# Kernel optimization log

Hardware: AMD Instinct MI355X
Metric: run time of the kernel (lower is better)

## Reference

```python
import jax, jax.numpy as jnp
import numpy as np

EMBED_DIM = 1024
NUM_HEADS = 16
HEAD_DIM = EMBED_DIM // NUM_HEADS


def setup_inputs() -> dict:
    key = jax.random.key(0)
    k1, k2, k3, k4, k5 = jax.random.split(key, 5)
    B, T, C = 4, 2048, EMBED_DIM
    scale = 1.0 / np.sqrt(C)
    return {
        "x": jax.random.normal(k1, (B, T, C), dtype=jnp.float32),
        "W_qkv": jax.random.normal(k2, (3 * C, C), dtype=jnp.float32) * scale,
        "b_qkv": jax.random.normal(k3, (3 * C,), dtype=jnp.float32) * 0.02,
        "W_proj": jax.random.normal(k4, (C, C), dtype=jnp.float32) * scale,
        "b_proj": jax.random.normal(k5, (C,), dtype=jnp.float32) * 0.02,
    }


def reference(x, W_qkv, b_qkv, W_proj, b_proj):
    B, T, C = x.shape
    H, D = NUM_HEADS, HEAD_DIM
    qkv = x @ W_qkv.T + b_qkv                      # [B,T,3C]
    q, k, v = jnp.split(qkv, 3, axis=-1)
    q = q.reshape(B, T, H, D).transpose(0, 2, 1, 3)  # [B,H,T,D]
    k = k.reshape(B, T, H, D).transpose(0, 2, 1, 3)
    v = v.reshape(B, T, H, D).transpose(0, 2, 1, 3)
    scores = jnp.einsum("bhqd,bhkd->bhqk", q, k) / np.sqrt(D)  # [B,H,T,T]
    causal = jnp.tril(jnp.ones((T, T), dtype=bool))
    scores = jnp.where(causal, scores, -jnp.inf)
    attn = jax.nn.softmax(scores, axis=-1)
    out = jnp.einsum("bhqk,bhkd->bhqd", attn, v)   # [B,H,T,D]
    out = out.transpose(0, 2, 1, 3).reshape(B, T, C)
    return out @ W_proj.T + b_proj
```

## Files before the change

### kernel.cpp

```cpp
#include <hip/hip_runtime.h>
#include <math.h>

#define EMBED 1024
#define NHEAD 16
#define HDIM  64
#define SEQT  2048
#define BATCH 4

typedef __bf16 bf16x4 __attribute__((ext_vector_type(4)));
typedef __bf16 bf16x8 __attribute__((ext_vector_type(8)));
typedef float  f32x4  __attribute__((ext_vector_type(4)));

#define AS1 __attribute__((address_space(1)))
#define AS3 __attribute__((address_space(3)))
#define GLD_LDS16(gp, lp) __builtin_amdgcn_global_load_lds( \
    (const AS1 unsigned int*)(gp), (AS3 unsigned int*)(lp), 16, 0, 0)

#define QSCALE 0.180336880f

__device__ __forceinline__ unsigned short f2bf_hw(float f) {
    union { __bf16 h; unsigned short u; } c; c.h = (__bf16)f; return c.u;
}

__global__ __launch_bounds__(256)
void cvt_all(const float* __restrict__ x, const float* __restrict__ wq,
             const float* __restrict__ wp,
             unsigned short* __restrict__ xb, unsigned short* __restrict__ wqb,
             unsigned short* __restrict__ wpb)
{
    const int N1 = 2097152;
    const int N2 = 786432;
    int i = blockIdx.x * 256 + threadIdx.x;
    const float4* src; ushort4* dst; int j;
    if (i < N1)            { src = (const float4*)x;  dst = (ushort4*)xb;  j = i; }
    else if (i < N1 + N2)  { src = (const float4*)wq; dst = (ushort4*)wqb; j = i - N1; }
    else                   { src = (const float4*)wp; dst = (ushort4*)wpb; j = i - N1 - N2; }
    float4 v = src[j];
    ushort4 o;
    o.x = f2bf_hw(v.x); o.y = f2bf_hw(v.y); o.z = f2bf_hw(v.z); o.w = f2bf_hw(v.w);
    dst[j] = o;
}

#define BAR do { __builtin_amdgcn_sched_barrier(0); \
                 __builtin_amdgcn_s_barrier(); \
                 __builtin_amdgcn_sched_barrier(0); } while (0)

template<int MODE>
__global__ __launch_bounds__(512, 2)
void gemm_bt_8ph(const unsigned short* __restrict__ A, const unsigned short* __restrict__ Bw,
                 const float* __restrict__ bias,
                 void* out0, void* out1, void* out2,
                 int M, int N, int K)
{
    __shared__ __align__(16) unsigned short Asm[2][256 * 64];
    __shared__ __align__(16) unsigned short Bsm[2][256 * 64];

    const int tid  = threadIdx.x;
    const int lane = tid & 63;
    const int wave = tid >> 6;
    const int wm = wave >> 2, wn = wave & 3;
    const int col = lane & 15, quad = lane >> 4;
    const long m0 = (long)blockIdx.y * 256, n0 = (long)blockIdx.x * 256;

    f32x4 acc[8][4];
#pragma unroll
    for (int mi = 0; mi < 8; mi++)
#pragma unroll
        for (int ni = 0; ni < 4; ni++) acc[mi][ni] = (f32x4){0.f, 0.f, 0.f, 0.f};

    const int srow  = tid >> 3;
    const int sslot = tid & 7;
    const int gslot = sslot ^ (srow & 7);
    const unsigned short* Agb = A  + (m0 + srow) * (long)K + gslot * 8;
    const unsigned short* Bgb = Bw + (n0 + srow) * (long)K + gslot * 8;

#define STAGE(b, kt_) do { const long ko_ = (long)(kt_) * 64; \
    _Pragma("unroll") for (int r_ = 0; r_ < 4; r_++) { \
        GLD_LDS16(Agb + (long)r_ * 64 * K + ko_, &Asm[b][0] + r_ * 4096 + tid * 8); \
        GLD_LDS16(Bgb + (long)r_ * 64 * K + ko_, &Bsm[b][0] + r_ * 4096 + tid * 8); \
    } } while (0)

#define LOAD_A(qm_) do { _Pragma("unroll") for (int i_ = 0; i_ < 4; i_++) { \
        const int row_ = wm * 128 + ((qm_) * 4 + i_) * 16 + col; \
        const int rx_ = row_ & 7; \
        af[i_][0] = *(const bf16x8*)&Ac[row_ * 64 + ((quad    ) ^ rx_) * 8]; \
        af[i_][1] = *(const bf16x8*)&Ac[row_ * 64 + ((quad + 4) ^ rx_) * 8]; \
    } } while (0)

#define LOAD_B(qn_) do { _Pragma("unroll") for (int j_ = 0; j_ < 2; j_++) { \
        const int row_ = wn * 64 + ((qn_) * 2 + j_) * 16 + col; \
        const int rx_ = row_ & 7; \
        bfv[j_][0] = *(const bf16x8*)&Bc[row_ * 64 + ((quad    ) ^ rx_) * 8]; \
        bfv[j_][1] = *(const bf16x8*)&Bc[row_ * 64 + ((quad + 4) ^ rx_) * 8]; \
    } } while (0)

#define MFMA_Q(qm_, qn_) do { __builtin_amdgcn_s_setprio(1); \
    _Pragma("unroll") for (int i_ = 0; i_ < 4; i_++) \
    _Pragma("unroll") for (int j_ = 0; j_ < 2; j_++) { \
        acc[(qm_) * 4 + i_][(qn_) * 2 + j_] = __builtin_amdgcn_mfma_f32_16x16x32_bf16( \
            af[i_][0], bfv[j_][0], acc[(qm_) * 4 + i_][(qn_) * 2 + j_], 0, 0, 0); \
        acc[(qm_) * 4 + i_][(qn_) * 2 + j_] = __builtin_amdgcn_mfma_f32_16x16x32_bf16( \
            af[i_][1], bfv[j_][1], acc[(qm_) * 4 + i_][(qn_) * 2 + j_], 0, 0, 0); \
    } \
    __builtin_amdgcn_s_setprio(0); } while (0)

    STAGE(0, 0);
    __builtin_amdgcn_s_waitcnt(0x0F70);
    BAR;

    const int T = K >> 6;
    for (int kt = 0; kt < T; kt++) {
        const int cur = kt & 1;
        const unsigned short* Ac = &Asm[cur][0];
        const unsigned short* Bc = &Bsm[cur][0];
        bf16x8 af[4][2], bfv[2][2];

        LOAD_A(0); LOAD_B(0);
        if (kt + 1 < T) STAGE(cur ^ 1, kt + 1);
        BAR;
        MFMA_Q(0, 0);
        BAR;
        LOAD_B(1);
        BAR;
        MFMA_Q(0, 1);
        BAR;
        LOAD_A(1);
        BAR;
        MFMA_Q(1, 1);
        BAR;
        LOAD_B(0);
        BAR;
        MFMA_Q(1, 0);
        __builtin_amdgcn_s_waitcnt(0x0F70);
        BAR;
    }

#undef STAGE
#undef LOAD_A
#undef LOAD_B
#undef MFMA_Q

#pragma unroll
    for (int mi = 0; mi < 8; mi++) {
#pragma unroll
        for (int ni = 0; ni < 4; ni++) {
            long n = n0 + wn * 64 + ni * 16 + col;
            float bv = bias[n];
#pragma unroll
            for (int r = 0; r < 4; r++) {
                long m = m0 + wm * 128 + mi * 16 + quad * 4 + r;
                float v = acc[mi][ni][r] + bv;
                if (MODE == 0) {
                    ((float*)out0)[m * N + n] = v;
                } else {
                    int which = (int)(n >> 10);
                    int c = (int)(n & 1023);
                    int h = c >> 6, d = c & 63;
                    int b = (int)(m >> 11), t = (int)(m & 2047);
                    long bh = (long)(b * NHEAD + h);
                    if (which == 0)      ((unsigned short*)out0)[(bh * SEQT + t) * HDIM + d] = f2bf_hw(v * QSCALE);
                    else if (which == 1) ((unsigned short*)out1)[(bh * SEQT + t) * HDIM + d] = f2bf_hw(v);
                    else                 ((unsigned short*)out2)[(bh * HDIM + d) * SEQT + t] = f2bf_hw(v);
                }
            }
        }
    }
}

#define PPAD 72

__global__ __launch_bounds__(256, 3)
void flash_attn_mfma4(const unsigned short* __restrict__ Qb,
                      const unsigned short* __restrict__ Kb,
                      const unsigned short* __restrict__ Vt,
                      unsigned short* __restrict__ Ob)
{
    __shared__ __align__(16) unsigned short P_lds[128 * PPAD];
    __shared__ __align__(16) unsigned short K_lds[2][64 * 64];
    __shared__ __align__(16) unsigned short V_lds[2][64 * 64];
    __shared__ __align__(16) float L_lds[128];

    const int tid  = threadIdx.x;
    const int lane = tid & 63;
    const int wave = tid >> 6;
    const int col  = lane & 15;
    const int quad = lane >> 4;

    const int idx = blockIdx.x;
    const int qt = 15 - (idx >> 6);
    const int hb = idx & 63;
    const int h = hb & 15, b = hb >> 4;
    const int q0 = qt * 128;
    const long bh = (long)(b * NHEAD + h);
    const unsigned short* Kbh = Kb + bh * SEQT * HDIM;
    const unsigned short* Vbh = Vt + bh * HDIM * SEQT;
    const int ktiles = 2 * qt + 2;

    const int r0 = tid >> 3,         c0 = (tid & 7) ^ (r0 & 7);
    const int r1 = (tid + 256) >> 3, c1 = (tid & 7) ^ (r1 & 7);

    bf16x8 qf[2][2];
#pragma unroll
    for (int ni = 0; ni < 2; ni++) {
        const unsigned short* qrow = Qb + (bh * SEQT + q0 + wave * 32 + ni * 16 + col) * HDIM;
        qf[ni][0] = *(const bf16x8*)(qrow + quad * 8);
        qf[ni][1] = *(const bf16x8*)(qrow + 32 + quad * 8);
    }

    GLD_LDS16(Kbh + r0 * HDIM + c0 * 8,        &K_lds[0][0] + tid * 8);
    GLD_LDS16(Kbh + r1 * HDIM + c1 * 8,        &K_lds[0][0] + 2048 + tid * 8);
    GLD_LDS16(Vbh + (long)r0 * SEQT + c0 * 8,  &V_lds[0][0] + tid * 8);
    GLD_LDS16(Vbh + (long)r1 * SEQT + c1 * 8,  &V_lds[0][0] + 2048 + tid * 8);

    f32x4 o[2][4];
#pragma unroll
    for (int mi = 0; mi < 2; mi++)
#pragma unroll
        for (int dt = 0; dt < 4; dt++) o[mi][dt] = (f32x4){0.f, 0.f, 0.f, 0.f};
    float rs[2] = {0.f, 0.f};

    const int cswz0 = quad ^ (col & 7);
    const int cswz1 = (quad + 4) ^ (col & 7);

    for (int kt = 0; kt < ktiles; kt++) {
        const int cur = kt & 1;
        __builtin_amdgcn_s_waitcnt(0x0F70);
        __syncthreads();
        if (kt + 1 < ktiles) {
            const int k0n = (kt + 1) * 64, nxt = cur ^ 1;
            GLD_LDS16(Kbh + (k0n + r0) * HDIM + c0 * 8,       &K_lds[nxt][0] + tid * 8);
            GLD_LDS16(Kbh + (k0n + r1) * HDIM + c1 * 8,       &K_lds[nxt][0] + 2048 + tid * 8);
            GLD_LDS16(Vbh + (long)r0 * SEQT + k0n + c0 * 8,   &V_lds[nxt][0] + tid * 8);
            GLD_LDS16(Vbh + (long)r1 * SEQT + k0n + c1 * 8,   &V_lds[nxt][0] + 2048 + tid * 8);
        }

        const unsigned short* Kc = &K_lds[cur][0];
        f32x4 st[4][2];
#pragma unroll
        for (int mt = 0; mt < 4; mt++) {
            const int row = mt * 16 + col;
            bf16x8 kf0 = *(const bf16x8*)&Kc[row * 64 + cswz0 * 8];
            bf16x8 kf1 = *(const bf16x8*)&Kc[row * 64 + cswz1 * 8];
#pragma unroll
            for (int ni = 0; ni < 2; ni++) {
                f32x4 acc = (f32x4){0.f, 0.f, 0.f, 0.f};
                acc = __builtin_amdgcn_mfma_f32_16x16x32_bf16(kf0, qf[ni][0], acc, 0, 0, 0);
                acc = __builtin_amdgcn_mfma_f32_16x16x32_bf16(kf1, qf[ni][1], acc, 0, 0, 0);
                st[mt][ni] = acc;
            }
        }
        const int k0 = kt * 64;
        if (kt >= 2 * qt) {
#pragma unroll
            for (int mt = 0; mt < 4; mt++) {
                const int keybase = k0 + mt * 16 + quad * 4;
#pragma unroll
                for (int ni = 0; ni < 2; ni++) {
                    const int qg = q0 + wave * 32 + ni * 16 + col;
#pragma unroll
                    for (int r = 0; r < 4; r++)
                        if (keybase + r > qg) st[mt][ni][r] = -INFINITY;
                }
            }
        }

#pragma unroll
        for (int mt = 0; mt < 4; mt++)
#pragma unroll
            for (int ni = 0; ni < 2; ni++) {
                f32x4 p;
#pragma unroll
                for (int r = 0; r < 4; r++) p[r] = __builtin_amdgcn_exp2f(st[mt][ni][r]);
                rs[ni] += (p[0] + p[1]) + (p[2] + p[3]);
                bf16x4 pb = __builtin_convertvector(p, bf16x4);
                *(bf16x4*)&P_lds[(wave * 32 + ni * 16 + col) * PPAD + mt * 16 + quad * 4] = pb;
            }

        const unsigned short* Vc = &V_lds[cur][0];
#pragma unroll
        for (int mi = 0; mi < 2; mi++) {
            const unsigned short* prow = &P_lds[(wave * 32 + mi * 16 + col) * PPAD];
            bf16x8 pf0 = *(const bf16x8*)(prow + quad * 8);
            bf16x8 pf1 = *(const bf16x8*)(prow + 32 + quad * 8);
#pragma unroll
            for (int dt = 0; dt < 4; dt++) {
                const int row = dt * 16 + col;
                bf16x8 vf0 = *(const bf16x8*)&Vc[row * 64 + cswz0 * 8];
                bf16x8 vf1 = *(const bf16x8*)&Vc[row * 64 + cswz1 * 8];
                o[mi][dt] = __builtin_amdgcn_mfma_f32_16x16x32_bf16(pf0, vf0, o[mi][dt], 0, 0, 0);
                o[mi][dt] = __builtin_amdgcn_mfma_f32_16x16x32_bf16(pf1, vf1, o[mi][dt], 0, 0, 0);
            }
        }
    }

#pragma unroll
    for (int ni = 0; ni < 2; ni++) {
        rs[ni] += __shfl_xor(rs[ni], 16);
        rs[ni] += __shfl_xor(rs[ni], 32);
        if (quad == 0) L_lds[wave * 32 + ni * 16 + col] = rs[ni];
    }
    __syncthreads();
    f32x4 lf[2];
#pragma unroll
    for (int mi = 0; mi < 2; mi++)
        lf[mi] = *(const f32x4*)&L_lds[wave * 32 + mi * 16 + quad * 4];

#pragma unroll
    for (int mi = 0; mi < 2; mi++)
#pragma unroll
        for (int r = 0; r < 4; r++) {
            float inv = 1.f / lf[mi][r];
            int t = q0 + wave * 32 + mi * 16 + quad * 4 + r;
            unsigned short* orow = Ob + ((long)(b * SEQT + t)) * EMBED + h * HDIM;
#pragma unroll
            for (int dt = 0; dt < 4; dt++)
                orow[dt * 16 + col] = f2bf_hw(o[mi][dt][r] * inv);
        }
}

extern "C" void kernel_launch(void* const* d_in, const int* in_sizes, int n_in,
                              void* d_out, int out_size, void* d_ws, size_t ws_size,
                              hipStream_t stream)
{
    const float* x     = (const float*)d_in[0];
    const float* Wqkv  = (const float*)d_in[1];
    const float* bqkv  = (const float*)d_in[2];
    const float* Wproj = (const float*)d_in[3];
    const float* bproj = (const float*)d_in[4];
    float* out = (float*)d_out;

    const long Mbt = (long)BATCH * SEQT;
    const long per = (long)BATCH * NHEAD * SEQT * HDIM;

    unsigned short* xb  = (unsigned short*)d_ws;
    unsigned short* wqb = xb  + per;
    unsigned short* wpb = wqb + 3 * EMBED * EMBED;
    unsigned short* Qb  = wpb + EMBED * EMBED;
    unsigned short* Kb  = Qb + per;
    unsigned short* Vt  = Kb + per;
    unsigned short* Ob  = Vt + per;

    cvt_all<<<12288, 256, 0, stream>>>(x, Wqkv, Wproj, xb, wqb, wpb);

    dim3 g1(3 * EMBED / 256, Mbt / 256);
    gemm_bt_8ph<1><<<g1, 512, 0, stream>>>(xb, wqb, bqkv, Qb, Kb, Vt,
                                           (int)Mbt, 3 * EMBED, EMBED);

    flash_attn_mfma4<<<1024, 256, 0, stream>>>(Qb, Kb, Vt, Ob);

    dim3 g3(EMBED / 256, Mbt / 256);
    gemm_bt_8ph<0><<<g3, 512, 0, stream>>>(Ob, wpb, bproj, out, nullptr, nullptr,
                                           (int)Mbt, EMBED, EMBED);
}
```

Before: 284.2 us.

## Rework GEMM as triple-buffered 256x128 tile pipeline with XCD-aware block remap

```diff
diff --git a/kernel.cpp b/kernel.cpp
--- a/kernel.cpp
+++ b/kernel.cpp
@@ -47,24 +47,32 @@
 
 template<int MODE>
 __global__ __launch_bounds__(512, 2)
-void gemm_bt_8ph(const unsigned short* __restrict__ A, const unsigned short* __restrict__ Bw,
-                 const float* __restrict__ bias,
-                 void* out0, void* out1, void* out2,
-                 int M, int N, int K)
+void gemm_bt_pipe(const unsigned short* __restrict__ A, const unsigned short* __restrict__ Bw,
+                  const float* __restrict__ bias,
+                  void* out0, void* out1, void* out2,
+                  int M, int N)
 {
-    __shared__ __align__(16) unsigned short Asm[2][256 * 64];
-    __shared__ __align__(16) unsigned short Bsm[2][256 * 64];
+    const int K = 1024;
+    const int T = 16;
+    __shared__ __align__(16) unsigned short Asm[3][256 * 64];
+    __shared__ __align__(16) unsigned short Bsm[3][128 * 64];
 
     const int tid  = threadIdx.x;
     const int lane = tid & 63;
     const int wave = tid >> 6;
-    const int wm = wave >> 2, wn = wave & 3;
+    const int wm = wave >> 1, wn = wave & 1;
     const int col = lane & 15, quad = lane >> 4;
-    const long m0 = (long)blockIdx.y * 256, n0 = (long)blockIdx.x * 256;
-
-    f32x4 acc[8][4];
-#pragma unroll
-    for (int mi = 0; mi < 8; mi++)
+
+    const int gx = gridDim.x;
+    const int nwg = gx * gridDim.y;
+    int wg = blockIdx.y * gx + blockIdx.x;
+    wg = (wg & 7) * (nwg >> 3) + (wg >> 3);
+    const long m0 = (long)(wg / gx) * 256;
+    const long n0 = (long)(wg % gx) * 128;
+
+    f32x4 acc[4][4];
+#pragma unroll
+    for (int mi = 0; mi < 4; mi++)
 #pragma unroll
         for (int ni = 0; ni < 4; ni++) acc[mi][ni] = (f32x4){0.f, 0.f, 0.f, 0.f};
 
@@ -74,81 +82,80 @@
     const unsigned short* Agb = A  + (m0 + srow) * (long)K + gslot * 8;
     const unsigned short* Bgb = Bw + (n0 + srow) * (long)K + gslot * 8;
 
-#define STAGE(b, kt_) do { const long ko_ = (long)(kt_) * 64; \
-    _Pragma("unroll") for (int r_ = 0; r_ < 4; r_++) { \
+#define STAGE_A(b, t_) do { const long ko_ = (long)(t_) * 64; \
+    _Pragma("unroll") for (int r_ = 0; r_ < 4; r_++) \
         GLD_LDS16(Agb + (long)r_ * 64 * K + ko_, &Asm[b][0] + r_ * 4096 + tid * 8); \
+    } while (0)
+#define STAGE_B(b, t_) do { const long ko_ = (long)(t_) * 64; \
+    _Pragma("unroll") for (int r_ = 0; r_ < 2; r_++) \
         GLD_LDS16(Bgb + (long)r_ * 64 * K + ko_, &Bsm[b][0] + r_ * 4096 + tid * 8); \
-    } } while (0)
-
-#define LOAD_A(qm_) do { _Pragma("unroll") for (int i_ = 0; i_ < 4; i_++) { \
-        const int row_ = wm * 128 + ((qm_) * 4 + i_) * 16 + col; \
+    } while (0)
+
+#define LOAD_A() do { _Pragma("unroll") for (int i_ = 0; i_ < 4; i_++) { \
+        const int row_ = wm * 64 + i_ * 16 + col; \
         const int rx_ = row_ & 7; \
         af[i_][0] = *(const bf16x8*)&Ac[row_ * 64 + ((quad    ) ^ rx_) * 8]; \
         af[i_][1] = *(const bf16x8*)&Ac[row_ * 64 + ((quad + 4) ^ rx_) * 8]; \
     } } while (0)
 
 #define LOAD_B(qn_) do { _Pragma("unroll") for (int j_ = 0; j_ < 2; j_++) { \
-        const int row_ = wn * 64 + ((qn_) * 2 + j_) * 16 + col; \
+        const int row_ = wn * 64 + (qn_) * 32 + j_ * 16 + col; \
         const int rx_ = row_ & 7; \
         bfv[j_][0] = *(const bf16x8*)&Bc[row_ * 64 + ((quad    ) ^ rx_) * 8]; \
         bfv[j_][1] = *(const bf16x8*)&Bc[row_ * 64 + ((quad + 4) ^ rx_) * 8]; \
     } } while (0)
 
-#define MFMA_Q(qm_, qn_) do { __builtin_amdgcn_s_setprio(1); \
+#define MFMA_Q(qn_) do { __builtin_amdgcn_s_setprio(1); \
     _Pragma("unroll") for (int i_ = 0; i_ < 4; i_++) \
     _Pragma("unroll") for (int j_ = 0; j_ < 2; j_++) { \
-        acc[(qm_) * 4 + i_][(qn_) * 2 + j_] = __builtin_amdgcn_mfma_f32_16x16x32_bf16( \
-            af[i_][0], bfv[j_][0], acc[(qm_) * 4 + i_][(qn_) * 2 + j_], 0, 0, 0); \
-        acc[(qm_) * 4 + i_][(qn_) * 2 + j_] = __builtin_amdgcn_mfma_f32_16x16x32_bf16( \
-            af[i_][1], bfv[j_][1], acc[(qm_) * 4 + i_][(qn_) * 2 + j_], 0, 0, 0); \
+        acc[i_][(qn_) * 2 + j_] = __builtin_amdgcn_mfma_f32_16x16x32_bf16( \
+            af[i_][0], bfv[j_][0], acc[i_][(qn_) * 2 + j_], 0, 0, 0); \
+        acc[i_][(qn_) * 2 + j_] = __builtin_amdgcn_mfma_f32_16x16x32_bf16( \
+            af[i_][1], bfv[j_][1], acc[i_][(qn_) * 2 + j_], 0, 0, 0); \
     } \
     __builtin_amdgcn_s_setprio(0); } while (0)
 
-    STAGE(0, 0);
-    __builtin_amdgcn_s_waitcnt(0x0F70);
+    STAGE_A(0, 0); STAGE_B(0, 0);
+    STAGE_A(1, 1); STAGE_B(1, 1);
+    __builtin_amdgcn_s_waitcnt(0x0F76);
     BAR;
 
-    const int T = K >> 6;
-    for (int kt = 0; kt < T; kt++) {
-        const int cur = kt & 1;
+#pragma unroll
+    for (int t = 0; t < T; t++) {
+        const int cur = t % 3, nb = (t + 2) % 3;
         const unsigned short* Ac = &Asm[cur][0];
         const unsigned short* Bc = &Bsm[cur][0];
         bf16x8 af[4][2], bfv[2][2];
 
-        LOAD_A(0); LOAD_B(0);
-        if (kt + 1 < T) STAGE(cur ^ 1, kt + 1);
+        LOAD_A(); LOAD_B(0);
+        if (t + 2 < T) STAGE_A(nb, t + 2);
         BAR;
-        MFMA_Q(0, 0);
+        MFMA_Q(0);
         BAR;
         LOAD_B(1);
+        if (t + 2 < T) STAGE_B(nb, t + 2);
         BAR;
-        MFMA_Q(0, 1);
+        MFMA_Q(1);
+        if (t + 2 < T)       __builtin_amdgcn_s_waitcnt(0x0F76);
+        else if (t + 2 == T) __builtin_amdgcn_s_waitcnt(0x0F70);
         BAR;
-        LOAD_A(1);
-        BAR;
-        MFMA_Q(1, 1);
-        BAR;
-        LOAD_B(0);
-        BAR;
-        MFMA_Q(1, 0);
-        __builtin_amdgcn_s_waitcnt(0x0F70);
-        BAR;
-    }
-
-#undef STAGE
+    }
+
+#undef STAGE_A
+#undef STAGE_B
 #undef LOAD_A
 #undef LOAD_B
 #undef MFMA_Q
 
 #pragma unroll
-    for (int mi = 0; mi < 8; mi++) {
+    for (int mi = 0; mi < 4; mi++) {
 #pragma unroll
         for (int ni = 0; ni < 4; ni++) {
             long n = n0 + wn * 64 + ni * 16 + col;
             float bv = bias[n];
 #pragma unroll
             for (int r = 0; r < 4; r++) {
-                long m = m0 + wm * 128 + mi * 16 + quad * 4 + r;
+                long m = m0 + wm * 64 + mi * 16 + quad * 4 + r;
                 float v = acc[mi][ni][r] + bv;
                 if (MODE == 0) {
                     ((float*)out0)[m * N + n] = v;
@@ -342,13 +349,13 @@
 
     cvt_all<<<12288, 256, 0, stream>>>(x, Wqkv, Wproj, xb, wqb, wpb);
 
-    dim3 g1(3 * EMBED / 256, Mbt / 256);
-    gemm_bt_8ph<1><<<g1, 512, 0, stream>>>(xb, wqb, bqkv, Qb, Kb, Vt,
-                                           (int)Mbt, 3 * EMBED, EMBED);
+    dim3 g1(3 * EMBED / 128, Mbt / 256);
+    gemm_bt_pipe<1><<<g1, 512, 0, stream>>>(xb, wqb, bqkv, Qb, Kb, Vt,
+                                            (int)Mbt, 3 * EMBED);
 
     flash_attn_mfma4<<<1024, 256, 0, stream>>>(Qb, Kb, Vt, Ob);
 
-    dim3 g3(EMBED / 256, Mbt / 256);
-    gemm_bt_8ph<0><<<g3, 512, 0, stream>>>(Ob, wpb, bproj, out, nullptr, nullptr,
-                                           (int)Mbt, EMBED, EMBED);
-}
+    dim3 g3(EMBED / 128, Mbt / 256);
+    gemm_bt_pipe<0><<<g3, 512, 0, stream>>>(Ob, wpb, bproj, out, nullptr, nullptr,
+                                            (int)Mbt, EMBED);
+}
```

After: 253.2 us. 1.12x faster.

## Split GEMM tile staging per quadrant and remap workgroups for locality

Applied to the files above, without the earlier changes.

```diff
diff --git a/kernel.cpp b/kernel.cpp
--- a/kernel.cpp
+++ b/kernel.cpp
@@ -47,11 +47,13 @@
 
 template<int MODE>
 __global__ __launch_bounds__(512, 2)
-void gemm_bt_8ph(const unsigned short* __restrict__ A, const unsigned short* __restrict__ Bw,
-                 const float* __restrict__ bias,
-                 void* out0, void* out1, void* out2,
-                 int M, int N, int K)
+void gemm_bt_m201(const unsigned short* __restrict__ A, const unsigned short* __restrict__ Bw,
+                  const float* __restrict__ bias,
+                  void* out0, void* out1, void* out2,
+                  int M, int N)
 {
+    const int K = 1024;
+    const int T = 16;
     __shared__ __align__(16) unsigned short Asm[2][256 * 64];
     __shared__ __align__(16) unsigned short Bsm[2][256 * 64];
 
@@ -60,7 +62,13 @@
     const int wave = tid >> 6;
     const int wm = wave >> 2, wn = wave & 3;
     const int col = lane & 15, quad = lane >> 4;
-    const long m0 = (long)blockIdx.y * 256, n0 = (long)blockIdx.x * 256;
+
+    const int gx = gridDim.x;
+    const int nwg = gx * gridDim.y;
+    int wg = blockIdx.y * gx + blockIdx.x;
+    wg = (wg & 7) * (nwg >> 3) + (wg >> 3);
+    const long m0 = (long)(wg / gx) * 256;
+    const long n0 = (long)(wg % gx) * 256;
 
     f32x4 acc[8][4];
 #pragma unroll
@@ -71,27 +79,30 @@
     const int srow  = tid >> 3;
     const int sslot = tid & 7;
     const int gslot = sslot ^ (srow & 7);
-    const unsigned short* Agb = A  + (m0 + srow) * (long)K + gslot * 8;
-    const unsigned short* Bgb = Bw + (n0 + srow) * (long)K + gslot * 8;
-
-#define STAGE(b, kt_) do { const long ko_ = (long)(kt_) * 64; \
-    _Pragma("unroll") for (int r_ = 0; r_ < 4; r_++) { \
-        GLD_LDS16(Agb + (long)r_ * 64 * K + ko_, &Asm[b][0] + r_ * 4096 + tid * 8); \
-        GLD_LDS16(Bgb + (long)r_ * 64 * K + ko_, &Bsm[b][0] + r_ * 4096 + tid * 8); \
+    const unsigned short* Agb = A + (m0 + srow) * (long)K + gslot * 8;
+    const unsigned short* Bgb = Bw + (n0 + (srow >> 5) * 64 + (srow & 31)) * (long)K + gslot * 8;
+
+#define STAGE_A(b, t_, qm_) do { \
+    GLD_LDS16(Agb + ((qm_) * 64      ) * (long)K + (t_) * 64, &Asm[b][((qm_) * 128     ) * 64] + tid * 8); \
+    GLD_LDS16(Agb + ((qm_) * 64 + 128) * (long)K + (t_) * 64, &Asm[b][((qm_) * 128 + 64) * 64] + tid * 8); \
+  } while (0)
+#define STAGE_B(b, t_, qn_) do { \
+    GLD_LDS16(Bgb + ((qn_) * 32      ) * (long)K + (t_) * 64, &Bsm[b][((qn_) * 128     ) * 64] + tid * 8); \
+    GLD_LDS16(Bgb + ((qn_) * 32 + 128) * (long)K + (t_) * 64, &Bsm[b][((qn_) * 128 + 64) * 64] + tid * 8); \
+  } while (0)
+
+#define LOAD_A(qm_) do { _Pragma("unroll") for (int i_ = 0; i_ < 4; i_++) { \
+        const int ra_ = (qm_) * 128 + wm * 64 + i_ * 16 + col; \
+        const int rx_ = col & 7; \
+        af[i_][0] = *(const bf16x8*)&Ac[ra_ * 64 + ((quad    ) ^ rx_) * 8]; \
+        af[i_][1] = *(const bf16x8*)&Ac[ra_ * 64 + ((quad + 4) ^ rx_) * 8]; \
     } } while (0)
 
-#define LOAD_A(qm_) do { _Pragma("unroll") for (int i_ = 0; i_ < 4; i_++) { \
-        const int row_ = wm * 128 + ((qm_) * 4 + i_) * 16 + col; \
-        const int rx_ = row_ & 7; \
-        af[i_][0] = *(const bf16x8*)&Ac[row_ * 64 + ((quad    ) ^ rx_) * 8]; \
-        af[i_][1] = *(const bf16x8*)&Ac[row_ * 64 + ((quad + 4) ^ rx_) * 8]; \
-    } } while (0)
-
 #define LOAD_B(qn_) do { _Pragma("unroll") for (int j_ = 0; j_ < 2; j_++) { \
-        const int row_ = wn * 64 + ((qn_) * 2 + j_) * 16 + col; \
-        const int rx_ = row_ & 7; \
-        bfv[j_][0] = *(const bf16x8*)&Bc[row_ * 64 + ((quad    ) ^ rx_) * 8]; \
-        bfv[j_][1] = *(const bf16x8*)&Bc[row_ * 64 + ((quad + 4) ^ rx_) * 8]; \
+        const int rb_ = (qn_) * 128 + wn * 32 + j_ * 16 + col; \
+        const int rx_ = col & 7; \
+        bfv[j_][0] = *(const bf16x8*)&Bc[rb_ * 64 + ((quad    ) ^ rx_) * 8]; \
+        bfv[j_][1] = *(const bf16x8*)&Bc[rb_ * 64 + ((quad + 4) ^ rx_) * 8]; \
     } } while (0)
 
 #define MFMA_Q(qm_, qn_) do { __builtin_amdgcn_s_setprio(1); \
@@ -104,38 +115,46 @@
     } \
     __builtin_amdgcn_s_setprio(0); } while (0)
 
-    STAGE(0, 0);
-    __builtin_amdgcn_s_waitcnt(0x0F70);
+    STAGE_A(0, 0, 0); STAGE_B(0, 0, 0); STAGE_B(0, 0, 1); STAGE_A(0, 0, 1);
+    __builtin_amdgcn_s_waitcnt(0x0F74);
     BAR;
 
-    const int T = K >> 6;
-    for (int kt = 0; kt < T; kt++) {
-        const int cur = kt & 1;
+#pragma unroll 2
+    for (int t = 0; t < T; t++) {
+        const int cur = t & 1, nb = cur ^ 1, nt = t + 1;
         const unsigned short* Ac = &Asm[cur][0];
         const unsigned short* Bc = &Bsm[cur][0];
         bf16x8 af[4][2], bfv[2][2];
 
         LOAD_A(0); LOAD_B(0);
-        if (kt + 1 < T) STAGE(cur ^ 1, kt + 1);
+        if (nt < T) STAGE_A(nb, nt, 0);
         BAR;
         MFMA_Q(0, 0);
+        if (nt < T) __builtin_amdgcn_s_waitcnt(0x0F74);
+        else        __builtin_amdgcn_s_waitcnt(0x0F72);
         BAR;
         LOAD_B(1);
+        if (nt < T) STAGE_B(nb, nt, 0);
         BAR;
         MFMA_Q(0, 1);
+        if (nt < T) __builtin_amdgcn_s_waitcnt(0x0F74);
+        else        __builtin_amdgcn_s_waitcnt(0x0F70);
         BAR;
         LOAD_A(1);
+        if (nt < T) STAGE_B(nb, nt, 1);
         BAR;
         MFMA_Q(1, 1);
         BAR;
         LOAD_B(0);
+        if (nt < T) STAGE_A(nb, nt, 1);
         BAR;
         MFMA_Q(1, 0);
-        __builtin_amdgcn_s_waitcnt(0x0F70);
-        BAR;
-    }
-
-#undef STAGE
+        if (nt < T) __builtin_amdgcn_s_waitcnt(0x0F74);
+        BAR;
+    }
+
+#undef STAGE_A
+#undef STAGE_B
 #undef LOAD_A
 #undef LOAD_B
 #undef MFMA_Q
@@ -343,12 +362,12 @@
     cvt_all<<<12288, 256, 0, stream>>>(x, Wqkv, Wproj, xb, wqb, wpb);
 
     dim3 g1(3 * EMBED / 256, Mbt / 256);
-    gemm_bt_8ph<1><<<g1, 512, 0, stream>>>(xb, wqb, bqkv, Qb, Kb, Vt,
-                                           (int)Mbt, 3 * EMBED, EMBED);
+    gemm_bt_m201<1><<<g1, 512, 0, stream>>>(xb, wqb, bqkv, Qb, Kb, Vt,
+                                            (int)Mbt, 3 * EMBED);
 
     flash_attn_mfma4<<<1024, 256, 0, stream>>>(Qb, Kb, Vt, Ob);
 
     dim3 g3(EMBED / 256, Mbt / 256);
-    gemm_bt_8ph<0><<<g3, 512, 0, stream>>>(Ob, wpb, bproj, out, nullptr, nullptr,
-                                           (int)Mbt, EMBED, EMBED);
-}
+    gemm_bt_m201<0><<<g3, 512, 0, stream>>>(Ob, wpb, bproj, out, nullptr, nullptr,
+                                            (int)Mbt, EMBED);
+}
```

Measured after the change: 281.5 us. No clear change (-0.9%).
